# Kernel optimization log

Hardware: AMD Instinct MI355X
Metric: run time of the kernel (lower is better)

Reference implementation:

```python
import jax, jax.numpy as jnp
import numpy as np

H_DIM = 1024
N_HEADS = 16
HEAD_D = H_DIM // N_HEADS  # 64


def setup_inputs() -> dict:
    key = jax.random.key(0)
    ks = jax.random.split(key, 10)
    B, T, C = 2, 2048, H_DIM
    init = 1.0 / np.sqrt(C)  # lecun_normal-scale stand-in
    src = jax.random.normal(ks[0], (B, T, C), dtype=jnp.float32)
    mask = jnp.ones((B, T), dtype=jnp.float32)  # unused when causal
    Wq = jax.random.normal(ks[1], (C, H_DIM), dtype=jnp.float32) * init
    Wk = jax.random.normal(ks[2], (C, H_DIM), dtype=jnp.float32) * init
    Wv = jax.random.normal(ks[3], (C, H_DIM), dtype=jnp.float32) * init
    Wo = jax.random.normal(ks[4], (H_DIM, H_DIM), dtype=jnp.float32) * init
    bq = jnp.zeros((H_DIM,), jnp.float32)
    bk = jnp.zeros((H_DIM,), jnp.float32)
    bv = jnp.zeros((H_DIM,), jnp.float32)
    bo = jnp.zeros((H_DIM,), jnp.float32)
    return {"src": src, "mask": mask, "Wq": Wq, "bq": bq, "Wk": Wk, "bk": bk,
            "Wv": Wv, "bv": bv, "Wo": Wo, "bo": bo}


def reference(src, mask, Wq, bq, Wk, bk, Wv, bv, Wo, bo):
    # MaskedCausalAttention forward, deterministic=True (dropout = identity),
    # use_causal_mask=True.
    B, T, C = src.shape
    N, D = N_HEADS, HEAD_D
    # q,k,v: [B, N, T, D]
    q = (src @ Wq + bq).reshape(B, T, N, D).transpose(0, 2, 1, 3)
    k = (src @ Wk + bk).reshape(B, T, N, D).transpose(0, 2, 1, 3)
    v = (src @ Wv + bv).reshape(B, T, N, D).transpose(0, 2, 1, 3)
    # scores: [B, N, T, T]
    scores = jnp.einsum('bntd,bnsd->bnts', q, k) / jnp.sqrt(jnp.float32(D))
    causal = jnp.tril(jnp.ones((T, T), dtype=bool))[None, None]
    scores = jnp.where(causal, scores, -jnp.inf)
    probs = jax.nn.softmax(scores, axis=-1)
    attn = jnp.einsum('bnts,bnsd->bntd', probs, v)  # [B, N, T, D]
    attn = attn.transpose(0, 2, 1, 3).reshape(B, T, N * D)
    return attn @ Wo + bo
```

## Files before the change

### kernel.cpp

```cpp
#include <hip/hip_runtime.h>
#include <hip/hip_bf16.h>

typedef __hip_bfloat16 bf16;
typedef __attribute__((ext_vector_type(8))) short short8;
typedef __attribute__((ext_vector_type(4))) float f32x4;

#define BATCH 2
#define SEQ   2048
#define HDIM  1024
#define NHEAD 16
#define DHEAD 64
#define MROWS (BATCH*SEQ)

#define QSCALE 0.18033688f
#define EXP2F(x) __builtin_amdgcn_exp2f(x)

static __device__ __forceinline__ short f2bs(float x) {
    __hip_bfloat16 h = (__hip_bfloat16)x;
    return *reinterpret_cast<short*>(&h);
}
static __device__ __forceinline__ unsigned int pk2(float a, float b) {
    __hip_bfloat162 h = __float22bfloat162_rn(make_float2(a, b));
    return *reinterpret_cast<unsigned int*>(&h);
}

static __device__ __forceinline__ void gload16(const void* g, void* l) {
    __builtin_amdgcn_global_load_lds(
        (const __attribute__((address_space(1))) unsigned int*)g,
        (__attribute__((address_space(3))) unsigned int*)l, 16, 0, 0);
}

__global__ __launch_bounds__(256) void prep1(const float* __restrict__ src,
        const float* __restrict__ Wq, const float* __restrict__ Wk,
        const float* __restrict__ Wv, const float* __restrict__ Wo,
        short* __restrict__ Sb, short* __restrict__ WT,
        short* __restrict__ WoT)
{
    __shared__ float t[64][65];
    const int bx = blockIdx.x, tid = threadIdx.x;
    if (bx < 4096) {
        int i = bx * 256 + tid;
        float4 v = ((const float4*)src)[i];
        ushort4 o;
        o.x = (unsigned short)f2bs(v.x);
        o.y = (unsigned short)f2bs(v.y);
        o.z = (unsigned short)f2bs(v.z);
        o.w = (unsigned short)f2bs(v.w);
        ((ushort4*)Sb)[i] = o;
        return;
    }
    const int tb = bx - 4096;
    const int wsel = tb >> 8;
    const float* W = (wsel == 0) ? Wq : (wsel == 1) ? Wk : (wsel == 2) ? Wv : Wo;
    short* dst = (wsel < 3) ? WT : WoT;
    const int roff = (wsel < 3) ? wsel * 1024 : 0;
    const int t8 = tb & 255;
    const int n0 = (t8 & 15) * 64, k0 = (t8 >> 4) * 64;
#pragma unroll
    for (int i = 0; i < 16; i++) {
        int idx = tid + i * 256, r = idx >> 6, c = idx & 63;
        t[r][c] = W[(size_t)(k0 + r) * HDIM + n0 + c];
    }
    __syncthreads();
#pragma unroll
    for (int i = 0; i < 16; i++) {
        int idx = tid + i * 256, c = idx >> 6, r = idx & 63;
        dst[(size_t)(roff + n0 + c) * HDIM + k0 + r] = f2bs(t[r][c]);
    }
}

__global__ __launch_bounds__(512, 2) void gemm_qkv(const short* __restrict__ A,
        const short* __restrict__ Bt,
        const float* __restrict__ bq, const float* __restrict__ bk,
        const float* __restrict__ bv,
        short* __restrict__ Qout, short* __restrict__ Kout,
        short* __restrict__ Vtout)
{
    __shared__ short SM[2][32768];
    const int tid = threadIdx.x, lane = tid & 63, w = tid >> 6;
    const int quad = lane >> 4, l15 = lane & 15;
    const int m0 = blockIdx.y * 256, n0 = blockIdx.x * 256;
    const int wr = w >> 1, wc = w & 1;

    const short* gp[4][2];
    int lo[4][2];
#pragma unroll
    for (int g = 0; g < 4; g++)
#pragma unroll
        for (int i = 0; i < 2; i++) {
            if (g < 2) {
                int u = g * 16 + w * 2 + i;
                gp[g][i] = A + (size_t)(m0 + (u >> 1) * 16 + l15) * HDIM
                             + (u & 1) * 32 + quad * 8;
                lo[g][i] = u * 512;
            } else {
                int j = w * 2 + i;
                int v = (g == 2 ? 0 : 8) + j + (j >= 8 ? 8 : 0);
                gp[g][i] = Bt + (size_t)(n0 + (v >> 1) * 16 + l15) * HDIM
                              + (v & 1) * 32 + quad * 8;
                lo[g][i] = 16384 + v * 512;
            }
        }

    f32x4 acc[4][8];
#pragma unroll
    for (int i = 0; i < 4; i++)
#pragma unroll
        for (int j = 0; j < 8; j++) acc[i][j] = (f32x4){0.f, 0.f, 0.f, 0.f};

#pragma unroll
    for (int g = 0; g < 4; g++)
#pragma unroll
        for (int i = 0; i < 2; i++) { gload16(gp[g][i], &SM[0][lo[g][i]]); gp[g][i] += 64; }
    asm volatile("s_waitcnt vmcnt(2)" ::: "memory");
    __builtin_amdgcn_s_barrier();

    short8 af[4][2];
    for (int t = 0; t < 16; ++t) {
        const short* Tb = SM[t & 1];
        short* Sn = SM[(t + 1) & 1];
#pragma unroll
        for (int p = 0; p < 4; ++p) {
            if (p == 0) {
#pragma unroll
                for (int mi = 0; mi < 4; mi++)
#pragma unroll
                    for (int kh = 0; kh < 2; kh++)
                        af[mi][kh] = *(const short8*)
                            &Tb[((wr * 4 + mi) * 2 + kh) * 512 + lane * 8];
            }
            short8 bfp[2][2];
#pragma unroll
            for (int n2 = 0; n2 < 2; n2++)
#pragma unroll
                for (int kh = 0; kh < 2; kh++)
                    bfp[n2][kh] = *(const short8*)
                        &Tb[16384 + ((wc * 8 + p * 2 + n2) * 2 + kh) * 512 + lane * 8];

            if (t < 15) {
                gload16(gp[p][0], Sn + lo[p][0]); gp[p][0] += 64;
                gload16(gp[p][1], Sn + lo[p][1]); gp[p][1] += 64;
                if (p == 1) asm volatile("s_waitcnt vmcnt(4)" ::: "memory");
                if (p == 3) asm volatile("s_waitcnt vmcnt(2)" ::: "memory");
            } else {
                if (p == 1) asm volatile("s_waitcnt vmcnt(0)" ::: "memory");
            }
            __builtin_amdgcn_s_barrier();
            __builtin_amdgcn_s_setprio(1);
#pragma unroll
            for (int n2 = 0; n2 < 2; n2++)
#pragma unroll
                for (int mi = 0; mi < 4; mi++)
#pragma unroll
                    for (int kh = 0; kh < 2; kh++)
                        acc[mi][p * 2 + n2] = __builtin_amdgcn_mfma_f32_16x16x32_bf16(
                            af[mi][kh], bfp[n2][kh], acc[mi][p * 2 + n2], 0, 0, 0);
            __builtin_amdgcn_s_setprio(0);
            __builtin_amdgcn_s_barrier();
        }
    }

    const int region = blockIdx.x >> 2;
    if (region < 2) {
        const float* bias = region ? bk : bq;
        const float oscale = region ? 1.0f : QSCALE;
        short* C = region ? Kout : Qout;
#pragma unroll
        for (int mi = 0; mi < 4; mi++) {
            int mB = m0 + wr * 64 + mi * 16 + quad * 4;
#pragma unroll
            for (int ni = 0; ni < 8; ni++) {
                int nl = (n0 + (wc * 8 + ni) * 16 + l15) & 1023;
                float bb = bias[nl];
#pragma unroll
                for (int r = 0; r < 4; r++)
                    C[(size_t)(mB + r) * HDIM + nl] =
                        f2bs((acc[mi][ni][r] + bb) * oscale);
            }
        }
    } else {
#pragma unroll
        for (int mi = 0; mi < 4; mi++) {
            int mB = m0 + wr * 64 + mi * 16 + quad * 4;
            int bb = mB >> 11, tt = mB & 2047;
#pragma unroll
            for (int ni = 0; ni < 8; ni++) {
                int n = n0 + (wc * 8 + ni) * 16 + l15;
                int h = (n >> 6) & 15, d = n & 63;
                float bvv = bv[n & 1023];
                size_t base = ((size_t)((bb * NHEAD + h) * DHEAD + d)) * SEQ + tt;
                ushort4 pk;
                pk.x = (unsigned short)f2bs(acc[mi][ni][0] + bvv);
                pk.y = (unsigned short)f2bs(acc[mi][ni][1] + bvv);
                pk.z = (unsigned short)f2bs(acc[mi][ni][2] + bvv);
                pk.w = (unsigned short)f2bs(acc[mi][ni][3] + bvv);
                *(ushort4*)(Vtout + base) = pk;
            }
        }
    }
}

__global__ __launch_bounds__(256) void attn_mfma(const short* __restrict__ Qb,
        const short* __restrict__ Kb, const short* __restrict__ Vt,
        short* __restrict__ Ab)
{
    __shared__ short SMEM[20992];
    const int tid = threadIdx.x, lane = tid & 63, w = tid >> 6;
    const int quad = lane >> 4, l15 = lane & 15;
    const int L = blockIdx.x;

    const int pair = (L & 7) + 8 * ((L >> 3) & 3);
    const int strip = 31 - (L >> 5);
    const int b = pair >> 4, head = pair & 15;

    const short* Kbh = Kb + (size_t)b * SEQ * HDIM + head * DHEAD;
    const short* Vth = Vt + (size_t)(b * NHEAD + head) * DHEAD * SEQ;
    short* Pw = SMEM + 16384 + w * 1152;

    const int qbase = strip * 64;
    const int qr = qbase + w * 16 + l15;

    const short* qptr = Qb + (size_t)(b * SEQ + qr) * HDIM + head * DHEAD + quad * 8;
    short8 bq0 = *(const short8*)qptr;
    short8 bq1 = *(const short8*)(qptr + 32);

    const short* gp[4];
    int stp[4], ldo[4];
#pragma unroll
    for (int i = 0; i < 4; i++) {
        int u = w * 4 + i;
        if (u < 8) {
            int t = u >> 1, h = u & 1;
            gp[i] = Kbh + (size_t)(t * 16 + l15) * HDIM + h * 32 + quad * 8;
            stp[i] = 64 * HDIM;
        } else {
            int c = u - 8, dt = c >> 1, kh = c & 1;
            gp[i] = Vth + (size_t)(dt * 16 + l15) * SEQ + kh * 32 + quad * 8;
            stp[i] = 64;
        }
        ldo[i] = u * 512;
    }

    f32x4 o[4];
#pragma unroll
    for (int dt = 0; dt < 4; dt++) o[dt] = (f32x4){0.f, 0.f, 0.f, 0.f};
    float psum = 0.f;

#pragma unroll
    for (int i = 0; i < 4; i++) { gload16(gp[i], &SMEM[ldo[i]]); gp[i] += stp[i]; }

    for (int it = 0; it <= strip; ++it) {
        const int cur = it & 1;
        short* Ks = &SMEM[cur * 8192];
        short* Vs = Ks + 4096;

        if (it < strip) {
            short* nb = &SMEM[(cur ^ 1) * 8192];
#pragma unroll
            for (int i = 0; i < 4; i++) { gload16(gp[i], nb + ldo[i]); gp[i] += stp[i]; }
            asm volatile("s_waitcnt vmcnt(4)" ::: "memory");
        } else {
            asm volatile("s_waitcnt vmcnt(0)" ::: "memory");
        }
        __builtin_amdgcn_s_barrier();
        const int s0 = it * 64;
        f32x4 sv[4];
        __builtin_amdgcn_s_setprio(1);
#pragma unroll
        for (int t = 0; t < 4; t++) {
            sv[t] = (f32x4){0.f, 0.f, 0.f, 0.f};
            short8 k0 = *(const short8*)&Ks[(t * 2) * 512 + lane * 8];
            short8 k1 = *(const short8*)&Ks[(t * 2 + 1) * 512 + lane * 8];
            sv[t] = __builtin_amdgcn_mfma_f32_16x16x32_bf16(k0, bq0, sv[t], 0, 0, 0);
            sv[t] = __builtin_amdgcn_mfma_f32_16x16x32_bf16(k1, bq1, sv[t], 0, 0, 0);
        }
        __builtin_amdgcn_s_setprio(0);

        float p[16];
        if (it == strip) {
#pragma unroll
            for (int t = 0; t < 4; t++)
#pragma unroll
                for (int r = 0; r < 4; r++) {
                    int key = s0 + t * 16 + quad * 4 + r;
                    p[t * 4 + r] = (key <= qr) ? EXP2F(sv[t][r]) : 0.f;
                }
        } else {
#pragma unroll
            for (int t = 0; t < 4; t++)
#pragma unroll
                for (int r = 0; r < 4; r++)
                    p[t * 4 + r] = EXP2F(sv[t][r]);
        }
#pragma unroll
        for (int i = 0; i < 16; i++) psum += p[i];

#pragma unroll
        for (int t = 0; t < 4; t++) {
            uint2 u2;
            u2.x = pk2(p[t * 4],     p[t * 4 + 1]);
            u2.y = pk2(p[t * 4 + 2], p[t * 4 + 3]);
            *(uint2*)&Pw[l15 * 72 + t * 16 + quad * 4] = u2;
        }
        short8 bp0 = *(const short8*)&Pw[l15 * 72 + quad * 8];
        short8 bp1 = *(const short8*)&Pw[l15 * 72 + 32 + quad * 8];

        __builtin_amdgcn_s_setprio(1);
#pragma unroll
        for (int dt = 0; dt < 4; dt++) {
            short8 av0 = *(const short8*)&Vs[(dt * 2) * 512 + lane * 8];
            short8 av1 = *(const short8*)&Vs[(dt * 2 + 1) * 512 + lane * 8];
            o[dt] = __builtin_amdgcn_mfma_f32_16x16x32_bf16(av0, bp0, o[dt], 0, 0, 0);
            o[dt] = __builtin_amdgcn_mfma_f32_16x16x32_bf16(av1, bp1, o[dt], 0, 0, 0);
        }
        __builtin_amdgcn_s_setprio(0);
        __builtin_amdgcn_s_barrier();
    }

    float lrow = psum + __shfl_xor(psum, 16);
    lrow += __shfl_xor(lrow, 32);
    const float inv = 1.f / lrow;

    const size_t obase = (size_t)(b * SEQ + qr) * HDIM + head * DHEAD;
#pragma unroll
    for (int dt = 0; dt < 4; dt++) {
        uint2 u2;
        u2.x = pk2(o[dt][0] * inv, o[dt][1] * inv);
        u2.y = pk2(o[dt][2] * inv, o[dt][3] * inv);
        *(uint2*)&Ab[obase + dt * 16 + quad * 4] = u2;
    }
}

__global__ __launch_bounds__(256) void gemm_o(const short* __restrict__ A,
        const short* __restrict__ Bt, const float* __restrict__ bo,
        float* __restrict__ Out)
{
    __shared__ short SM[2 * 12288];
    const int tid = threadIdx.x, lane = tid & 63, w = tid >> 6;
    const int quad = lane >> 4, l15 = lane & 15;
    const int m0 = blockIdx.y * 64, n0 = blockIdx.x * 128;
    const int wr = w >> 1, wc = w & 1;

    const short* gsrc[6];
    short* ldst[6];
#pragma unroll
    for (int i = 0; i < 6; i++) {
        int u = w * 6 + i;
        if (u < 8) {
            int mi = u >> 1, kh = u & 1;
            gsrc[i] = A + (size_t)(m0 + mi * 16 + l15) * HDIM + kh * 32 + quad * 8;
            ldst[i] = &SM[u * 512];
        } else {
            int v = u - 8, ni = v >> 1, kh = v & 1;
            gsrc[i] = Bt + (size_t)(n0 + ni * 16 + l15) * HDIM + kh * 32 + quad * 8;
            ldst[i] = &SM[4096 + v * 512];
        }
    }

    f32x4 acc[2][4];
#pragma unroll
    for (int i = 0; i < 2; i++)
#pragma unroll
        for (int j = 0; j < 4; j++) acc[i][j] = (f32x4){0.f, 0.f, 0.f, 0.f};

#pragma unroll
    for (int i = 0; i < 6; i++) { gload16(gsrc[i], ldst[i]); gsrc[i] += 64; }

    for (int kk = 0; kk < 16; ++kk) {
        const int cur = kk & 1;
        if (kk < 15) {
            const int nb = (cur ^ 1) * 12288;
#pragma unroll
            for (int i = 0; i < 6; i++) { gload16(gsrc[i], ldst[i] + nb); gsrc[i] += 64; }
            asm volatile("s_waitcnt vmcnt(6)" ::: "memory");
        } else {
            asm volatile("s_waitcnt vmcnt(0)" ::: "memory");
        }
        __builtin_amdgcn_s_barrier();

        const short* Asb = &SM[cur * 12288];
        const short* Bsb = Asb + 4096;
#pragma unroll
        for (int kh = 0; kh < 2; kh++) {
            short8 af[2], bfr[4];
#pragma unroll
            for (int mi = 0; mi < 2; mi++)
                af[mi] = *(const short8*)&Asb[((wr * 2 + mi) * 2 + kh) * 512 + lane * 8];
#pragma unroll
            for (int ni = 0; ni < 4; ni++)
                bfr[ni] = *(const short8*)&Bsb[((wc * 4 + ni) * 2 + kh) * 512 + lane * 8];
#pragma unroll
            for (int mi = 0; mi < 2; mi++)
#pragma unroll
                for (int ni = 0; ni < 4; ni++)
                    acc[mi][ni] = __builtin_amdgcn_mfma_f32_16x16x32_bf16(
                                      af[mi], bfr[ni], acc[mi][ni], 0, 0, 0);
        }
        __builtin_amdgcn_s_barrier();
    }

#pragma unroll
    for (int mi = 0; mi < 2; mi++) {
        int mB = m0 + (wr * 2 + mi) * 16 + quad * 4;
#pragma unroll
        for (int ni = 0; ni < 4; ni++) {
            int n = n0 + (wc * 4 + ni) * 16 + l15;
            float bb = bo[n];
#pragma unroll
            for (int r = 0; r < 4; r++)
                Out[(size_t)(mB + r) * HDIM + n] = acc[mi][ni][r] + bb;
        }
    }
}

extern "C" void kernel_launch(void* const* d_in, const int* in_sizes, int n_in,
                              void* d_out, int out_size, void* d_ws, size_t ws_size,
                              hipStream_t stream)
{
    const float* src = (const float*)d_in[0];
    const float* Wq = (const float*)d_in[2];
    const float* bq = (const float*)d_in[3];
    const float* Wk = (const float*)d_in[4];
    const float* bk = (const float*)d_in[5];
    const float* Wv = (const float*)d_in[6];
    const float* bv = (const float*)d_in[7];
    const float* Wo = (const float*)d_in[8];
    const float* bo = (const float*)d_in[9];
    float* out = (float*)d_out;

    short* Sb   = (short*)d_ws;
    short* Qb   = Sb + (size_t)MROWS * HDIM;
    short* Kb   = Qb + (size_t)MROWS * HDIM;
    short* Vt   = Kb + (size_t)MROWS * HDIM;
    short* WoT  = Vt + (size_t)MROWS * HDIM;
    short* WT   = (short*)d_out;
    short* Ab   = Qb;

    prep1<<<dim3(4096 + 1024), dim3(256), 0, stream>>>(src, Wq, Wk, Wv, Wo, Sb, WT, WoT);

    gemm_qkv<<<dim3(12, 16), dim3(512), 0, stream>>>(Sb, WT, bq, bk, bv, Qb, Kb, Vt);

    attn_mfma<<<dim3(1024), dim3(256), 0, stream>>>(Qb, Kb, Vt, Ab);

    gemm_o<<<dim3(8, 64), dim3(256), 0, stream>>>(Ab, WoT, bo, out);
}
```

Baseline: 203.7 us.

## Split long causal attention strips across two blocks and retile output GEMM

The longest half of the causal query strips (strips 16-31) are split into two key-range halves, each handled by its own block. The partial unnormalized outputs and row sums go to scratch buffers, and a new combine kernel merges them into the bf16 attention output. This aims to even out per-block work and reduce tail imbalance, at the cost of an extra launch and fp32 scratch traffic. The output-projection GEMM also moves to 128x128 tiles with 512 threads, for more reuse per block and fewer blocks.

```diff
diff --git a/kernel.cpp b/kernel.cpp
--- a/kernel.cpp
+++ b/kernel.cpp
@@ -202,7 +202,8 @@
 
 __global__ __launch_bounds__(256) void attn_mfma(const short* __restrict__ Qb,
         const short* __restrict__ Kb, const short* __restrict__ Vt,
-        short* __restrict__ Ab)
+        short* __restrict__ Ab,
+        float* __restrict__ Opart, float* __restrict__ Psum)
 {
     __shared__ short SMEM[20992];
     const int tid = threadIdx.x, lane = tid & 63, w = tid >> 6;
@@ -210,15 +211,24 @@
     const int L = blockIdx.x;
 
     const int pair = (L & 7) + 8 * ((L >> 3) & 3);
-    const int strip = 31 - (L >> 5);
+    const int u = L >> 5;
     const int b = pair >> 4, head = pair & 15;
+    int s, it0, itEnd, half, split;
+    if (u < 32) {
+        split = 1; s = 31 - (u >> 1); half = u & 1;
+        int mid = (s + 2) >> 1;
+        it0 = half ? mid : 0;
+        itEnd = half ? (s + 1) : mid;
+    } else {
+        split = 0; s = 47 - u; half = 0; it0 = 0; itEnd = s + 1;
+    }
+    const int nj = itEnd - it0;
 
     const short* Kbh = Kb + (size_t)b * SEQ * HDIM + head * DHEAD;
     const short* Vth = Vt + (size_t)(b * NHEAD + head) * DHEAD * SEQ;
     short* Pw = SMEM + 16384 + w * 1152;
 
-    const int qbase = strip * 64;
-    const int qr = qbase + w * 16 + l15;
+    const int qr = s * 64 + w * 16 + l15;
 
     const short* qptr = Qb + (size_t)(b * SEQ + qr) * HDIM + head * DHEAD + quad * 8;
     short8 bq0 = *(const short8*)qptr;
@@ -228,17 +238,18 @@
     int stp[4], ldo[4];
 #pragma unroll
     for (int i = 0; i < 4; i++) {
-        int u = w * 4 + i;
-        if (u < 8) {
-            int t = u >> 1, h = u & 1;
+        int c8 = w * 4 + i;
+        if (c8 < 8) {
+            int t = c8 >> 1, h = c8 & 1;
             gp[i] = Kbh + (size_t)(t * 16 + l15) * HDIM + h * 32 + quad * 8;
             stp[i] = 64 * HDIM;
         } else {
-            int c = u - 8, dt = c >> 1, kh = c & 1;
+            int c = c8 - 8, dt = c >> 1, kh = c & 1;
             gp[i] = Vth + (size_t)(dt * 16 + l15) * SEQ + kh * 32 + quad * 8;
             stp[i] = 64;
         }
-        ldo[i] = u * 512;
+        ldo[i] = c8 * 512;
+        gp[i] += (size_t)it0 * stp[i];
     }
 
     f32x4 o[4];
@@ -249,12 +260,12 @@
 #pragma unroll
     for (int i = 0; i < 4; i++) { gload16(gp[i], &SMEM[ldo[i]]); gp[i] += stp[i]; }
 
-    for (int it = 0; it <= strip; ++it) {
-        const int cur = it & 1;
+    for (int j = 0; j < nj; ++j) {
+        const int cur = j & 1;
         short* Ks = &SMEM[cur * 8192];
         short* Vs = Ks + 4096;
 
-        if (it < strip) {
+        if (j + 1 < nj) {
             short* nb = &SMEM[(cur ^ 1) * 8192];
 #pragma unroll
             for (int i = 0; i < 4; i++) { gload16(gp[i], nb + ldo[i]); gp[i] += stp[i]; }
@@ -263,7 +274,8 @@
             asm volatile("s_waitcnt vmcnt(0)" ::: "memory");
         }
         __builtin_amdgcn_s_barrier();
-        const int s0 = it * 64;
+        const int itg = it0 + j;
+        const int s0 = itg * 64;
         f32x4 sv[4];
         __builtin_amdgcn_s_setprio(1);
 #pragma unroll
@@ -277,7 +289,7 @@
         __builtin_amdgcn_s_setprio(0);
 
         float p[16];
-        if (it == strip) {
+        if (itg == s) {
 #pragma unroll
             for (int t = 0; t < 4; t++)
 #pragma unroll
@@ -319,8 +331,19 @@
 
     float lrow = psum + __shfl_xor(psum, 16);
     lrow += __shfl_xor(lrow, 32);
+
+    if (split) {
+        const int tile = (pair * 16 + (s - 16)) * 2 + half;
+        float* Ot = Opart + (size_t)tile * 4096;
+        const int rho = w * 16 + l15;
+#pragma unroll
+        for (int dt = 0; dt < 4; dt++)
+            *(f32x4*)&Ot[rho * 64 + dt * 16 + quad * 4] = o[dt];
+        if (quad == 0) Psum[tile * 64 + rho] = lrow;
+        return;
+    }
+
     const float inv = 1.f / lrow;
-
     const size_t obase = (size_t)(b * SEQ + qr) * HDIM + head * DHEAD;
 #pragma unroll
     for (int dt = 0; dt < 4; dt++) {
@@ -331,68 +354,99 @@
     }
 }
 
-__global__ __launch_bounds__(256) void gemm_o(const short* __restrict__ A,
+__global__ __launch_bounds__(256) void combine(const float* __restrict__ Opart,
+        const float* __restrict__ Psum, short* __restrict__ Ab)
+{
+    const int bxx = blockIdx.x;
+    const int pair = bxx & 31, sidx = bxx >> 5;
+    const int b = pair >> 4, head = pair & 15;
+    const int s = 16 + sidx;
+    const int tid = threadIdx.x;
+    const int row = tid >> 2, dq = (tid & 3) * 16;
+
+    const size_t t0 = ((size_t)(pair * 16 + sidx) * 2) * 4096;
+    const float* O0 = Opart + t0;
+    const float* O1 = O0 + 4096;
+    const int p0 = (pair * 16 + sidx) * 2 * 64;
+    const float inv = 1.f / (Psum[p0 + row] + Psum[p0 + 64 + row]);
+
+    const size_t obase = (size_t)(b * SEQ + s * 64 + row) * HDIM + head * DHEAD + dq;
+#pragma unroll
+    for (int g = 0; g < 4; g++) {
+        float4 a = *(const float4*)&O0[row * 64 + dq + g * 4];
+        float4 c = *(const float4*)&O1[row * 64 + dq + g * 4];
+        ushort4 pk;
+        pk.x = (unsigned short)f2bs((a.x + c.x) * inv);
+        pk.y = (unsigned short)f2bs((a.y + c.y) * inv);
+        pk.z = (unsigned short)f2bs((a.z + c.z) * inv);
+        pk.w = (unsigned short)f2bs((a.w + c.w) * inv);
+        *(ushort4*)&Ab[obase + g * 4] = pk;
+    }
+}
+
+__global__ __launch_bounds__(512) void gemm_o(const short* __restrict__ A,
         const short* __restrict__ Bt, const float* __restrict__ bo,
         float* __restrict__ Out)
 {
-    __shared__ short SM[2 * 12288];
+    __shared__ short SM[2 * 16384];
     const int tid = threadIdx.x, lane = tid & 63, w = tid >> 6;
     const int quad = lane >> 4, l15 = lane & 15;
-    const int m0 = blockIdx.y * 64, n0 = blockIdx.x * 128;
-    const int wr = w >> 1, wc = w & 1;
-
-    const short* gsrc[6];
-    short* ldst[6];
-#pragma unroll
-    for (int i = 0; i < 6; i++) {
-        int u = w * 6 + i;
-        if (u < 8) {
-            int mi = u >> 1, kh = u & 1;
-            gsrc[i] = A + (size_t)(m0 + mi * 16 + l15) * HDIM + kh * 32 + quad * 8;
-            ldst[i] = &SM[u * 512];
+    const int m0 = blockIdx.y * 128, n0 = blockIdx.x * 128;
+    const int wr = w >> 2, wc = w & 3;
+
+    const short* gsrc[4];
+    short* ldst[4];
+#pragma unroll
+    for (int i = 0; i < 4; i++) {
+        int c8 = w * 4 + i;
+        if (c8 < 16) {
+            gsrc[i] = A + (size_t)(m0 + (c8 >> 1) * 16 + l15) * HDIM
+                        + (c8 & 1) * 32 + quad * 8;
+            ldst[i] = &SM[c8 * 512];
         } else {
-            int v = u - 8, ni = v >> 1, kh = v & 1;
-            gsrc[i] = Bt + (size_t)(n0 + ni * 16 + l15) * HDIM + kh * 32 + quad * 8;
-            ldst[i] = &SM[4096 + v * 512];
-        }
-    }
-
-    f32x4 acc[2][4];
-#pragma unroll
-    for (int i = 0; i < 2; i++)
-#pragma unroll
-        for (int j = 0; j < 4; j++) acc[i][j] = (f32x4){0.f, 0.f, 0.f, 0.f};
-
-#pragma unroll
-    for (int i = 0; i < 6; i++) { gload16(gsrc[i], ldst[i]); gsrc[i] += 64; }
+            int v = c8 - 16;
+            gsrc[i] = Bt + (size_t)(n0 + (v >> 1) * 16 + l15) * HDIM
+                         + (v & 1) * 32 + quad * 8;
+            ldst[i] = &SM[8192 + v * 512];
+        }
+    }
+
+    f32x4 acc[4][2];
+#pragma unroll
+    for (int i = 0; i < 4; i++)
+#pragma unroll
+        for (int j = 0; j < 2; j++) acc[i][j] = (f32x4){0.f, 0.f, 0.f, 0.f};
+
+#pragma unroll
+    for (int i = 0; i < 4; i++) { gload16(gsrc[i], ldst[i]); gsrc[i] += 64; }
 
     for (int kk = 0; kk < 16; ++kk) {
         const int cur = kk & 1;
         if (kk < 15) {
-            const int nb = (cur ^ 1) * 12288;
-#pragma unroll
-            for (int i = 0; i < 6; i++) { gload16(gsrc[i], ldst[i] + nb); gsrc[i] += 64; }
-            asm volatile("s_waitcnt vmcnt(6)" ::: "memory");
+            const int nb = (cur ^ 1) * 16384;
+#pragma unroll
+            for (int i = 0; i < 4; i++) { gload16(gsrc[i], ldst[i] + nb); gsrc[i] += 64; }
+            asm volatile("s_waitcnt vmcnt(4)" ::: "memory");
         } else {
             asm volatile("s_waitcnt vmcnt(0)" ::: "memory");
         }
         __builtin_amdgcn_s_barrier();
 
-        const short* Asb = &SM[cur * 12288];
-        const short* Bsb = Asb + 4096;
+        const short* Asb = &SM[cur * 16384];
+        const short* Bsb = Asb + 8192;
 #pragma unroll
         for (int kh = 0; kh < 2; kh++) {
-            short8 af[2], bfr[4];
-#pragma unroll
-            for (int mi = 0; mi < 2; mi++)
-                af[mi] = *(const short8*)&Asb[((wr * 2 + mi) * 2 + kh) * 512 + lane * 8];
-#pragma unroll
-            for (int ni = 0; ni < 4; ni++)
-                bfr[ni] = *(const short8*)&Bsb[((wc * 4 + ni) * 2 + kh) * 512 + lane * 8];
-#pragma unroll
-            for (int mi = 0; mi < 2; mi++)
-#pragma unroll
-                for (int ni = 0; ni < 4; ni++)
+            short8 af[4], bfr[2];
+#pragma unroll
+            for (int mi = 0; mi < 4; mi++)
+                af[mi] = *(const short8*)&Asb[((wr * 4 + mi) * 2 + kh) * 512 + lane * 8];
+#pragma unroll
+            for (int ni = 0; ni < 2; ni++)
+                bfr[ni] = *(const short8*)&Bsb[((wc * 2 + ni) * 2 + kh) * 512 + lane * 8];
+#pragma unroll
+            for (int mi = 0; mi < 4; mi++)
+#pragma unroll
+                for (int ni = 0; ni < 2; ni++)
                     acc[mi][ni] = __builtin_amdgcn_mfma_f32_16x16x32_bf16(
                                       af[mi], bfr[ni], acc[mi][ni], 0, 0, 0);
         }
@@ -400,11 +454,11 @@
     }
 
 #pragma unroll
-    for (int mi = 0; mi < 2; mi++) {
-        int mB = m0 + (wr * 2 + mi) * 16 + quad * 4;
-#pragma unroll
-        for (int ni = 0; ni < 4; ni++) {
-            int n = n0 + (wc * 4 + ni) * 16 + l15;
+    for (int mi = 0; mi < 4; mi++) {
+        int mB = m0 + (wr * 4 + mi) * 16 + quad * 4;
+#pragma unroll
+        for (int ni = 0; ni < 2; ni++) {
+            int n = n0 + (wc * 2 + ni) * 16 + l15;
             float bb = bo[n];
 #pragma unroll
             for (int r = 0; r < 4; r++)
@@ -435,12 +489,16 @@
     short* WoT  = Vt + (size_t)MROWS * HDIM;
     short* WT   = (short*)d_out;
     short* Ab   = Qb;
+    float* Opart = (float*)d_out;
+    float* Psum  = (float*)Sb;
 
     prep1<<<dim3(4096 + 1024), dim3(256), 0, stream>>>(src, Wq, Wk, Wv, Wo, Sb, WT, WoT);
 
     gemm_qkv<<<dim3(12, 16), dim3(512), 0, stream>>>(Sb, WT, bq, bk, bv, Qb, Kb, Vt);
 
-    attn_mfma<<<dim3(1024), dim3(256), 0, stream>>>(Qb, Kb, Vt, Ab);
-
-    gemm_o<<<dim3(8, 64), dim3(256), 0, stream>>>(Ab, WoT, bo, out);
-}
+    attn_mfma<<<dim3(1536), dim3(256), 0, stream>>>(Qb, Kb, Vt, Ab, Opart, Psum);
+
+    combine<<<dim3(512), dim3(256), 0, stream>>>(Opart, Psum, Ab);
+
+    gemm_o<<<dim3(8, 32), dim3(512), 0, stream>>>(Ab, WoT, bo, out);
+}
```

Result: no change. 203.8 us (+0.0%).
